# Performance work log

Measured on AMD Instinct MI355X. Metric: run time of the kernel, lower is better.

## Reference

```python
import jax, jax.numpy as jnp
import numpy as np

H = 512  # hidden_size


def setup_inputs() -> dict:
    key = jax.random.key(0)
    ks = jax.random.split(key, 7)
    B, T, I = 256, 512, 3
    s = 1.0 / np.sqrt(H)
    return {
        "x": jax.random.normal(ks[0], (B, T, I), dtype=jnp.float32),
        "W_ih": jax.random.uniform(ks[1], (4 * H, I), dtype=jnp.float32, minval=-s, maxval=s),
        "W_hh": jax.random.uniform(ks[2], (4 * H, H), dtype=jnp.float32, minval=-s, maxval=s),
        "b_ih": jax.random.uniform(ks[3], (4 * H,), dtype=jnp.float32, minval=-s, maxval=s),
        "b_hh": jax.random.uniform(ks[4], (4 * H,), dtype=jnp.float32, minval=-s, maxval=s),
        "fc_w": jax.random.uniform(ks[5], (1, H), dtype=jnp.float32, minval=-s, maxval=s),
        "fc_b": jax.random.uniform(ks[6], (1,), dtype=jnp.float32, minval=-s, maxval=s),
    }


def _lstm_last_h(x, W_ih, W_hh, b_ih, b_hh):
    B = x.shape[0]
    # precompute input contribution for all timesteps: [B, T, 4H]
    x_gates = jnp.einsum('bti,gi->btg', x, W_ih) + (b_ih + b_hh)
    h0 = jnp.zeros((B, H), dtype=x.dtype)
    c0 = jnp.zeros((B, H), dtype=x.dtype)

    def step(carry, xg):
        h, c = carry
        gates = xg + h @ W_hh.T  # [B, 4H]
        i, f, g, o = jnp.split(gates, 4, axis=-1)  # torch order: i, f, g, o
        i = jax.nn.sigmoid(i)
        f = jax.nn.sigmoid(f)
        g = jnp.tanh(g)
        o = jax.nn.sigmoid(o)
        c_new = f * c + i * g
        h_new = o * jnp.tanh(c_new)
        return (h_new, c_new), None

    (h_last, _), _ = jax.lax.scan(step, (h0, c0), jnp.swapaxes(x_gates, 0, 1))
    return h_last  # [B, H]


def reference(x, W_ih, W_hh, b_ih, b_hh, fc_w, fc_b):
    h_last = _lstm_last_h(x, W_ih, W_hh, b_ih, b_hh)
    return h_last @ fc_w.T + fc_b  # [B, 1]
```

## Files before the change

kernel.cpp:

```cpp
#include <hip/hip_runtime.h>


#define Hh   512
#define Bsz  256
#define Tt   512

#define MB   32
#define HS   16
#define NROW 64
#define NTHR 512
#define NWG  256

typedef float    f32x4 __attribute__((ext_vector_type(4)));
typedef _Float16 f16x8 __attribute__((ext_vector_type(8)));
typedef unsigned long long u64;

#define PLANE_ELE (Bsz * Hh)
#define PLANES   3
#define BAR_OFF  (PLANES * PLANE_ELE * 2)
#define CTRL_UINTS 4096

__device__ __forceinline__ float sigm(float v)  { return 1.0f / (1.0f + __expf(-v)); }
__device__ __forceinline__ float tanhx(float v) { return 2.0f / (1.0f + __expf(-2.0f * v)) - 1.0f; }

__device__ __forceinline__ ushort f2h(float f) {
  return __builtin_bit_cast(ushort, (_Float16)f);
}
__device__ __forceinline__ float h2f(ushort u) {
  return (float)__builtin_bit_cast(_Float16, u);
}

#define GLOAD(dst, base, imm)                                            \
  asm volatile("global_load_dwordx4 %0, %1, off offset:%c2 sc0 sc1"      \
               : "=v"(dst) : "v"(base), "i"(imm))

__global__ void init_ws(unsigned* ctrl) {
  for (int i = threadIdx.x; i < CTRL_UINTS; i += NTHR) ctrl[i] = 0u;
}

__global__ __launch_bounds__(NTHR, 2)
void lstm_kernel(const float* __restrict__ x,   const float* __restrict__ Wih,
                 const float* __restrict__ Whh, const float* __restrict__ bih,
                 const float* __restrict__ bhh, const float* __restrict__ fcw,
                 const float* __restrict__ fcb, float* __restrict__ out,
                 char* __restrict__ ws)
{
  const int tid = threadIdx.x;
  const int wg  = blockIdx.x;
  const int bb  = wg & 7;
  const int hb  = wg >> 3;
  const int j0  = hb * HS;
  const int b0  = bb * MB;

  ushort*   hpl   = (ushort*)ws;
  unsigned* flags = (unsigned*)(ws + BAR_OFF) + bb * 512;

  __shared__ ushort whiF[4 * 16 * 64 * 8];
  __shared__ ushort wloF[4 * 16 * 64 * 8];
  __shared__ float  gates2[2][4][MB][20];
  __shared__ float  wih_s[NROW][3];
  __shared__ float  bsum[NROW];
  __shared__ float  xs[MB][3];

  if (tid < NROW) {
    int qq = tid >> 4, jj = tid & 15;
    int grow = qq * Hh + j0 + jj;
    wih_s[tid][0] = Wih[grow * 3 + 0];
    wih_s[tid][1] = Wih[grow * 3 + 1];
    wih_s[tid][2] = Wih[grow * 3 + 2];
    bsum[tid] = bih[grow] + bhh[grow];
  }

  for (int idx = tid; idx < NROW * 64; idx += NTHR) {
    int row = idx >> 6, seg = idx & 63;
    int qq = row >> 4, jj = row & 15;
    const float* src = Whh + (size_t)(qq * Hh + j0 + jj) * Hh + seg * 8;
    float4 w0 = *(const float4*)(src);
    float4 w1 = *(const float4*)(src + 4);
    float wv[8] = {w0.x, w0.y, w0.z, w0.w, w1.x, w1.y, w1.z, w1.w};
    unsigned uhi[4], ulo[4];
    #pragma unroll
    for (int p = 0; p < 4; ++p) {
      ushort h0 = f2h(wv[2*p]);
      ushort h1 = f2h(wv[2*p+1]);
      ushort l0 = f2h((wv[2*p]   - h2f(h0)) * 1024.0f);
      ushort l1 = f2h((wv[2*p+1] - h2f(h1)) * 1024.0f);
      uhi[p] = (unsigned)h0 | ((unsigned)h1 << 16);
      ulo[p] = (unsigned)l0 | ((unsigned)l1 << 16);
    }
    int kblk = seg >> 2, lkk = seg & 3;
    int dst = ((qq * 16 + kblk) * 64 + lkk * 16 + jj) * 8;
    *(uint4*)&whiF[dst] = make_uint4(uhi[0], uhi[1], uhi[2], uhi[3]);
    *(uint4*)&wloF[dst] = make_uint4(ulo[0], ulo[1], ulo[2], ulo[3]);
  }

  {
    int b = tid >> 4, jj = tid & 15;
    size_t o = (size_t)(b0 + b) * Hh + j0 + jj;
    __hip_atomic_store(&hpl[o], (ushort)0, __ATOMIC_RELAXED, __HIP_MEMORY_SCOPE_AGENT);
  }
  asm volatile("s_waitcnt vmcnt(0)" ::: "memory");
  __syncthreads();
  if (tid == 0) {
    unsigned fv = 1u;
    asm volatile("global_store_dword %0, %1, off sc0 sc1"
                 :: "v"(flags + hb * 16), "v"(fv) : "memory");
  }

  const int l   = tid & 63;
  const int wid = tid >> 6;
  const int m   = wid >> 2;
  const int ks  = wid & 3;
  const int lm  = l & 15;
  const int lk  = l >> 4;

  const size_t aoff = (size_t)(b0 + m * 16 + lm) * Hh + ks * 128 + lk * 8;
  const int    wq0  = ks * 2048 + l * 8;

  const int cb = tid >> 4;
  const int cj = tid & 15;
  float c_state = 0.0f;

  int rd = 0, wr = 1;
  for (int t = 0; t < Tt; ++t) {
    {
      const unsigned tq = (unsigned)(t + 1);
      const unsigned tw = (unsigned)t;
      if (wid == 0) {
        unsigned v = 0xFFFFFFFFu;
        const unsigned* fp = flags + (l & 31) * 16;
        for (;;) {
          if (l < 32)
            asm volatile("global_load_dword %0, %1, off sc0 sc1" : "=v"(v) : "v"(fp) : "memory");
          asm volatile("s_waitcnt vmcnt(0)" ::: "memory");
          unsigned need = ((l & 31) < 8) ? tq : tw;
          if (__all((int)(v >= need))) break;
          __builtin_amdgcn_s_sleep(2);
        }
      } else {
        unsigned v = 0xFFFFFFFFu;
        const unsigned* fp = flags + (ks * 8 + (l & 7)) * 16;
        for (;;) {
          if (l < 8)
            asm volatile("global_load_dword %0, %1, off sc0 sc1" : "=v"(v) : "v"(fp) : "memory");
          asm volatile("s_waitcnt vmcnt(0)" ::: "memory");
          if (__all((int)(v >= tq))) break;
          __builtin_amdgcn_s_sleep(2);
        }
      }
    }

    if (tid < MB * 3) {
      int b = tid / 3, ii = tid - b * 3;
      xs[b][ii] = x[(size_t)(b0 + b) * (Tt * 3) + t * 3 + ii];
    }

    const char* pH = (const char*)(hpl + (size_t)rd * PLANE_ELE + aoff);
    f32x4 AH[4];
    GLOAD(AH[0], pH, 0);  GLOAD(AH[1], pH, 64);  GLOAD(AH[2], pH, 128); GLOAD(AH[3], pH, 192);
    asm volatile("s_waitcnt vmcnt(0)" ::: "memory");
    __builtin_amdgcn_sched_barrier(0);

    f32x4 h0 = {0,0,0,0}, h1 = {0,0,0,0}, h2 = {0,0,0,0}, h3 = {0,0,0,0};
    f32x4 l0 = {0,0,0,0}, l1 = {0,0,0,0}, l2 = {0,0,0,0}, l3 = {0,0,0,0};
    #pragma unroll
    for (int u = 0; u < 4; ++u) {
      f16x8 ah = __builtin_bit_cast(f16x8, AH[u]);
      const int fo = wq0 + u * 512;
      {
        f16x8 bh = *(const f16x8*)&whiF[0 * 8192 + fo];
        f16x8 bl = *(const f16x8*)&wloF[0 * 8192 + fo];
        h0 = __builtin_amdgcn_mfma_f32_16x16x32_f16(ah, bh, h0, 0, 0, 0);
        l0 = __builtin_amdgcn_mfma_f32_16x16x32_f16(ah, bl, l0, 0, 0, 0);
      }
      {
        f16x8 bh = *(const f16x8*)&whiF[1 * 8192 + fo];
        f16x8 bl = *(const f16x8*)&wloF[1 * 8192 + fo];
        h1 = __builtin_amdgcn_mfma_f32_16x16x32_f16(ah, bh, h1, 0, 0, 0);
        l1 = __builtin_amdgcn_mfma_f32_16x16x32_f16(ah, bl, l1, 0, 0, 0);
      }
      {
        f16x8 bh = *(const f16x8*)&whiF[2 * 8192 + fo];
        f16x8 bl = *(const f16x8*)&wloF[2 * 8192 + fo];
        h2 = __builtin_amdgcn_mfma_f32_16x16x32_f16(ah, bh, h2, 0, 0, 0);
        l2 = __builtin_amdgcn_mfma_f32_16x16x32_f16(ah, bl, l2, 0, 0, 0);
      }
      {
        f16x8 bh = *(const f16x8*)&whiF[3 * 8192 + fo];
        f16x8 bl = *(const f16x8*)&wloF[3 * 8192 + fo];
        h3 = __builtin_amdgcn_mfma_f32_16x16x32_f16(ah, bh, h3, 0, 0, 0);
        l3 = __builtin_amdgcn_mfma_f32_16x16x32_f16(ah, bl, l3, 0, 0, 0);
      }
    }
    const float ls = 1.0f / 1024.0f;
    f32x4 acc0 = h0 + l0 * ls;
    f32x4 acc1 = h1 + l1 * ls;
    f32x4 acc2 = h2 + l2 * ls;
    f32x4 acc3 = h3 + l3 * ls;

    const int rrow = m * 16 + lk * 4;
    if (ks < 2) {
      #pragma unroll
      for (int r = 0; r < 4; ++r) {
        gates2[ks][0][rrow + r][lm] = acc0[r];
        gates2[ks][1][rrow + r][lm] = acc1[r];
        gates2[ks][2][rrow + r][lm] = acc2[r];
        gates2[ks][3][rrow + r][lm] = acc3[r];
      }
    }
    __syncthreads();
    if (ks >= 2) {
      #pragma unroll
      for (int r = 0; r < 4; ++r) {
        gates2[ks - 2][0][rrow + r][lm] += acc0[r];
        gates2[ks - 2][1][rrow + r][lm] += acc1[r];
        gates2[ks - 2][2][rrow + r][lm] += acc2[r];
        gates2[ks - 2][3][rrow + r][lm] += acc3[r];
      }
    }
    __syncthreads();

    {
      float xv0 = xs[cb][0], xv1 = xs[cb][1], xv2 = xs[cb][2];
      float pre[4];
      #pragma unroll
      for (int qq = 0; qq < 4; ++qq) {
        int r = qq * 16 + cj;
        pre[qq] = gates2[0][qq][cb][cj] + gates2[1][qq][cb][cj] + bsum[r]
                + xv0 * wih_s[r][0] + xv1 * wih_s[r][1] + xv2 * wih_s[r][2];
      }
      float ig = sigm(pre[0]), fg = sigm(pre[1]);
      float gg = tanhx(pre[2]), og = sigm(pre[3]);
      c_state = fg * c_state + ig * gg;
      float hv = og * tanhx(c_state);
      unsigned uhw = f2h(hv);
      size_t ho = (size_t)wr * PLANE_ELE + (size_t)(b0 + cb) * Hh + j0 + cj;
      asm volatile("global_store_short %0, %1, off sc0 sc1" :: "v"(hpl + ho), "v"(uhw));
    }

    asm volatile("s_waitcnt vmcnt(0)" ::: "memory");
    __syncthreads();
    if (tid == 0) {
      unsigned fv = (unsigned)(t + 2);
      asm volatile("global_store_dword %0, %1, off sc0 sc1"
                   :: "v"(flags + hb * 16), "v"(fv) : "memory");
    }

    rd = wr;
    wr = (wr == 2) ? 0 : wr + 1;
  }

  if (hb == 0) {
    if (tid < 64) {
      unsigned v = 0xFFFFFFFFu;
      const unsigned* fp = flags + (l & 31) * 16;
      const unsigned tgt = (unsigned)(Tt + 1);
      for (;;) {
        if (l < 32)
          asm volatile("global_load_dword %0, %1, off sc0 sc1" : "=v"(v) : "v"(fp) : "memory");
        asm volatile("s_waitcnt vmcnt(0)" ::: "memory");
        if (__all((int)(v >= tgt))) break;
        __builtin_amdgcn_s_sleep(2);
      }
    }
    __syncthreads();

    const u64* Hf = (const u64*)(hpl + (size_t)rd * PLANE_ELE);
    int b = tid >> 4, lj = tid & 15;
    float p = 0.0f;
    for (int jq = lj; jq < Hh / 4; jq += 16) {
      size_t o = (size_t)(b0 + b) * (Hh / 4) + jq;
      u64 uh = __hip_atomic_load(Hf + o, __ATOMIC_RELAXED, __HIP_MEMORY_SCOPE_AGENT);
      #pragma unroll
      for (int e = 0; e < 4; ++e)
        p += h2f((ushort)(uh >> (16 * e))) * fcw[4 * jq + e];
    }
    __syncthreads();
    ((float*)gates2)[tid] = p;
    __syncthreads();
    if (lj == 0) {
      float s = 0.0f;
      #pragma unroll
      for (int r = 0; r < 16; ++r) s += ((float*)gates2)[(b << 4) + r];
      out[b0 + b] = s + fcb[0];
    }
  }
}

extern "C" void kernel_launch(void* const* d_in, const int* in_sizes, int n_in,
                              void* d_out, int out_size, void* d_ws, size_t ws_size,
                              hipStream_t stream) {
  const float* x   = (const float*)d_in[0];
  const float* Wih = (const float*)d_in[1];
  const float* Whh = (const float*)d_in[2];
  const float* bih = (const float*)d_in[3];
  const float* bhh = (const float*)d_in[4];
  const float* fcw = (const float*)d_in[5];
  const float* fcb = (const float*)d_in[6];
  float* out = (float*)d_out;
  char*  ws  = (char*)d_ws;

  hipLaunchKernelGGL(init_ws, dim3(1), dim3(NTHR), 0, stream,
                     (unsigned*)(ws + BAR_OFF));
  hipLaunchKernelGGL(lstm_kernel, dim3(NWG), dim3(NTHR), 0, stream,
                     x, Wih, Whh, bih, bhh, fcw, fcb, out, ws);
}
```

Before: 1.834 ms.

## Keep W_hh fragments in registers, drop split-fp16 low part, retile to 16x32

Retiles the persistent LSTM grid from 8 batch groups x 32 hidden slices to 16 batch groups x 16 hidden slices of 32 units each. The recurrent weights now live as single fp16 MFMA fragments in each thread's registers instead of hi/lo fp16 pairs in LDS. This halves the MFMA count and removes the per-step LDS weight reads. Each wave handles a K-slice of 64 and the partial results are reduced through LDS across 8 waves. Dropping the low-order weight correction lowers accuracy, and the larger register footprint may hurt occupancy or cause spills.

```diff
diff --git a/kernel.cpp b/kernel.cpp
--- a/kernel.cpp
+++ b/kernel.cpp
@@ -5,9 +5,9 @@
 #define Bsz  256
 #define Tt   512
 
-#define MB   32
-#define HS   16
-#define NROW 64
+#define MB   16
+#define HS   32
+#define NROW 128
 #define NTHR 512
 #define NWG  256
 
@@ -23,11 +23,11 @@
 __device__ __forceinline__ float sigm(float v)  { return 1.0f / (1.0f + __expf(-v)); }
 __device__ __forceinline__ float tanhx(float v) { return 2.0f / (1.0f + __expf(-2.0f * v)) - 1.0f; }
 
+__device__ __forceinline__ float h2f(ushort u) {
+  return (float)__builtin_bit_cast(_Float16, u);
+}
 __device__ __forceinline__ ushort f2h(float f) {
   return __builtin_bit_cast(ushort, (_Float16)f);
-}
-__device__ __forceinline__ float h2f(ushort u) {
-  return (float)__builtin_bit_cast(_Float16, u);
 }
 
 #define GLOAD(dst, base, imm)                                            \
@@ -47,23 +47,21 @@
 {
   const int tid = threadIdx.x;
   const int wg  = blockIdx.x;
-  const int bb  = wg & 7;
-  const int hb  = wg >> 3;
+  const int bb  = wg & 15;
+  const int hb  = wg >> 4;
   const int j0  = hb * HS;
   const int b0  = bb * MB;
 
   ushort*   hpl   = (ushort*)ws;
-  unsigned* flags = (unsigned*)(ws + BAR_OFF) + bb * 512;
-
-  __shared__ ushort whiF[4 * 16 * 64 * 8];
-  __shared__ ushort wloF[4 * 16 * 64 * 8];
-  __shared__ float  gates2[2][4][MB][20];
-  __shared__ float  wih_s[NROW][3];
-  __shared__ float  bsum[NROW];
-  __shared__ float  xs[MB][3];
+  unsigned* flags = (unsigned*)(ws + BAR_OFF) + bb * 256;
+
+  __shared__ float gates2[4][NROW][17];
+  __shared__ float wih_s[NROW][3];
+  __shared__ float bsum[NROW];
+  __shared__ float xs[MB][3];
 
   if (tid < NROW) {
-    int qq = tid >> 4, jj = tid & 15;
+    int qq = tid >> 5, jj = tid & 31;
     int grow = qq * Hh + j0 + jj;
     wih_s[tid][0] = Wih[grow * 3 + 0];
     wih_s[tid][1] = Wih[grow * 3 + 1];
@@ -71,32 +69,34 @@
     bsum[tid] = bih[grow] + bhh[grow];
   }
 
-  for (int idx = tid; idx < NROW * 64; idx += NTHR) {
-    int row = idx >> 6, seg = idx & 63;
-    int qq = row >> 4, jj = row & 15;
-    const float* src = Whh + (size_t)(qq * Hh + j0 + jj) * Hh + seg * 8;
-    float4 w0 = *(const float4*)(src);
-    float4 w1 = *(const float4*)(src + 4);
-    float wv[8] = {w0.x, w0.y, w0.z, w0.w, w1.x, w1.y, w1.z, w1.w};
-    unsigned uhi[4], ulo[4];
+  const int l   = tid & 63;
+  const int ks  = tid >> 6;
+  const int lm  = l & 15;
+  const int lk  = l >> 4;
+
+  f16x8 wfrag[8][2];
+  #pragma unroll
+  for (int rb = 0; rb < 8; ++rb) {
     #pragma unroll
-    for (int p = 0; p < 4; ++p) {
-      ushort h0 = f2h(wv[2*p]);
-      ushort h1 = f2h(wv[2*p+1]);
-      ushort l0 = f2h((wv[2*p]   - h2f(h0)) * 1024.0f);
-      ushort l1 = f2h((wv[2*p+1] - h2f(h1)) * 1024.0f);
-      uhi[p] = (unsigned)h0 | ((unsigned)h1 << 16);
-      ulo[p] = (unsigned)l0 | ((unsigned)l1 << 16);
-    }
-    int kblk = seg >> 2, lkk = seg & 3;
-    int dst = ((qq * 16 + kblk) * 64 + lkk * 16 + jj) * 8;
-    *(uint4*)&whiF[dst] = make_uint4(uhi[0], uhi[1], uhi[2], uhi[3]);
-    *(uint4*)&wloF[dst] = make_uint4(ulo[0], ulo[1], ulo[2], ulo[3]);
+    for (int kb = 0; kb < 2; ++kb) {
+      int rr = rb * 16 + lm;
+      int grow = (rr >> 5) * Hh + j0 + (rr & 31);
+      int col = (ks * 2 + kb) * 32 + lk * 8;
+      const float* wsrc = Whh + (size_t)grow * Hh + col;
+      float4 wa = *(const float4*)(wsrc);
+      float4 wb = *(const float4*)(wsrc + 4);
+      f16x8 f;
+      f[0] = (_Float16)wa.x; f[1] = (_Float16)wa.y;
+      f[2] = (_Float16)wa.z; f[3] = (_Float16)wa.w;
+      f[4] = (_Float16)wb.x; f[5] = (_Float16)wb.y;
+      f[6] = (_Float16)wb.z; f[7] = (_Float16)wb.w;
+      wfrag[rb][kb] = f;
+    }
   }
 
   {
-    int b = tid >> 4, jj = tid & 15;
-    size_t o = (size_t)(b0 + b) * Hh + j0 + jj;
+    int cb0 = tid >> 5, cj0 = tid & 31;
+    size_t o = (size_t)(b0 + cb0) * Hh + j0 + cj0;
     __hip_atomic_store(&hpl[o], (ushort)0, __ATOMIC_RELAXED, __HIP_MEMORY_SCOPE_AGENT);
   }
   asm volatile("s_waitcnt vmcnt(0)" ::: "memory");
@@ -107,18 +107,10 @@
                  :: "v"(flags + hb * 16), "v"(fv) : "memory");
   }
 
-  const int l   = tid & 63;
-  const int wid = tid >> 6;
-  const int m   = wid >> 2;
-  const int ks  = wid & 3;
-  const int lm  = l & 15;
-  const int lk  = l >> 4;
-
-  const size_t aoff = (size_t)(b0 + m * 16 + lm) * Hh + ks * 128 + lk * 8;
-  const int    wq0  = ks * 2048 + l * 8;
-
-  const int cb = tid >> 4;
-  const int cj = tid & 15;
+  const size_t aoff = (size_t)(b0 + lm) * Hh + ks * 64 + lk * 8;
+
+  const int cb = tid >> 5;
+  const int cj = tid & 31;
   float c_state = 0.0f;
 
   int rd = 0, wr = 1;
@@ -126,22 +118,22 @@
     {
       const unsigned tq = (unsigned)(t + 1);
       const unsigned tw = (unsigned)t;
-      if (wid == 0) {
+      if (ks == 0) {
         unsigned v = 0xFFFFFFFFu;
-        const unsigned* fp = flags + (l & 31) * 16;
+        const unsigned* fp = flags + (l & 15) * 16;
         for (;;) {
-          if (l < 32)
+          if (l < 16)
             asm volatile("global_load_dword %0, %1, off sc0 sc1" : "=v"(v) : "v"(fp) : "memory");
           asm volatile("s_waitcnt vmcnt(0)" ::: "memory");
-          unsigned need = ((l & 31) < 8) ? tq : tw;
+          unsigned need = ((l & 15) < 2) ? tq : tw;
           if (__all((int)(v >= need))) break;
           __builtin_amdgcn_s_sleep(2);
         }
       } else {
         unsigned v = 0xFFFFFFFFu;
-        const unsigned* fp = flags + (ks * 8 + (l & 7)) * 16;
+        const unsigned* fp = flags + (ks * 2 + (l & 1)) * 16;
         for (;;) {
-          if (l < 8)
+          if (l < 2)
             asm volatile("global_load_dword %0, %1, off sc0 sc1" : "=v"(v) : "v"(fp) : "memory");
           asm volatile("s_waitcnt vmcnt(0)" ::: "memory");
           if (__all((int)(v >= tq))) break;
@@ -156,67 +148,36 @@
     }
 
     const char* pH = (const char*)(hpl + (size_t)rd * PLANE_ELE + aoff);
-    f32x4 AH[4];
-    GLOAD(AH[0], pH, 0);  GLOAD(AH[1], pH, 64);  GLOAD(AH[2], pH, 128); GLOAD(AH[3], pH, 192);
+    f32x4 AH[2];
+    GLOAD(AH[0], pH, 0);  GLOAD(AH[1], pH, 64);
     asm volatile("s_waitcnt vmcnt(0)" ::: "memory");
     __builtin_amdgcn_sched_barrier(0);
 
-    f32x4 h0 = {0,0,0,0}, h1 = {0,0,0,0}, h2 = {0,0,0,0}, h3 = {0,0,0,0};
-    f32x4 l0 = {0,0,0,0}, l1 = {0,0,0,0}, l2 = {0,0,0,0}, l3 = {0,0,0,0};
+    f32x4 acc[8];
     #pragma unroll
-    for (int u = 0; u < 4; ++u) {
-      f16x8 ah = __builtin_bit_cast(f16x8, AH[u]);
-      const int fo = wq0 + u * 512;
-      {
-        f16x8 bh = *(const f16x8*)&whiF[0 * 8192 + fo];
-        f16x8 bl = *(const f16x8*)&wloF[0 * 8192 + fo];
-        h0 = __builtin_amdgcn_mfma_f32_16x16x32_f16(ah, bh, h0, 0, 0, 0);
-        l0 = __builtin_amdgcn_mfma_f32_16x16x32_f16(ah, bl, l0, 0, 0, 0);
-      }
-      {
-        f16x8 bh = *(const f16x8*)&whiF[1 * 8192 + fo];
-        f16x8 bl = *(const f16x8*)&wloF[1 * 8192 + fo];
-        h1 = __builtin_amdgcn_mfma_f32_16x16x32_f16(ah, bh, h1, 0, 0, 0);
-        l1 = __builtin_amdgcn_mfma_f32_16x16x32_f16(ah, bl, l1, 0, 0, 0);
-      }
-      {
-        f16x8 bh = *(const f16x8*)&whiF[2 * 8192 + fo];
-        f16x8 bl = *(const f16x8*)&wloF[2 * 8192 + fo];
-        h2 = __builtin_amdgcn_mfma_f32_16x16x32_f16(ah, bh, h2, 0, 0, 0);
-        l2 = __builtin_amdgcn_mfma_f32_16x16x32_f16(ah, bl, l2, 0, 0, 0);
-      }
-      {
-        f16x8 bh = *(const f16x8*)&whiF[3 * 8192 + fo];
-        f16x8 bl = *(const f16x8*)&wloF[3 * 8192 + fo];
-        h3 = __builtin_amdgcn_mfma_f32_16x16x32_f16(ah, bh, h3, 0, 0, 0);
-        l3 = __builtin_amdgcn_mfma_f32_16x16x32_f16(ah, bl, l3, 0, 0, 0);
-      }
-    }
-    const float ls = 1.0f / 1024.0f;
-    f32x4 acc0 = h0 + l0 * ls;
-    f32x4 acc1 = h1 + l1 * ls;
-    f32x4 acc2 = h2 + l2 * ls;
-    f32x4 acc3 = h3 + l3 * ls;
-
-    const int rrow = m * 16 + lk * 4;
-    if (ks < 2) {
-      #pragma unroll
-      for (int r = 0; r < 4; ++r) {
-        gates2[ks][0][rrow + r][lm] = acc0[r];
-        gates2[ks][1][rrow + r][lm] = acc1[r];
-        gates2[ks][2][rrow + r][lm] = acc2[r];
-        gates2[ks][3][rrow + r][lm] = acc3[r];
-      }
-    }
-    __syncthreads();
-    if (ks >= 2) {
-      #pragma unroll
-      for (int r = 0; r < 4; ++r) {
-        gates2[ks - 2][0][rrow + r][lm] += acc0[r];
-        gates2[ks - 2][1][rrow + r][lm] += acc1[r];
-        gates2[ks - 2][2][rrow + r][lm] += acc2[r];
-        gates2[ks - 2][3][rrow + r][lm] += acc3[r];
-      }
+    for (int rb = 0; rb < 8; ++rb) acc[rb] = (f32x4){0.f, 0.f, 0.f, 0.f};
+    #pragma unroll
+    for (int kb = 0; kb < 2; ++kb) {
+      f16x8 ah = __builtin_bit_cast(f16x8, AH[kb]);
+      #pragma unroll
+      for (int rb = 0; rb < 8; ++rb)
+        acc[rb] = __builtin_amdgcn_mfma_f32_16x16x32_f16(ah, wfrag[rb][kb], acc[rb], 0, 0, 0);
+    }
+
+    if (ks < 4) {
+      #pragma unroll
+      for (int rb = 0; rb < 8; ++rb)
+        #pragma unroll
+        for (int r = 0; r < 4; ++r)
+          gates2[ks][rb * 16 + lm][lk * 4 + r] = acc[rb][r];
+    }
+    __syncthreads();
+    if (ks >= 4) {
+      #pragma unroll
+      for (int rb = 0; rb < 8; ++rb)
+        #pragma unroll
+        for (int r = 0; r < 4; ++r)
+          gates2[ks - 4][rb * 16 + lm][lk * 4 + r] += acc[rb][r];
     }
     __syncthreads();
 
@@ -225,9 +186,10 @@
       float pre[4];
       #pragma unroll
       for (int qq = 0; qq < 4; ++qq) {
-        int r = qq * 16 + cj;
-        pre[qq] = gates2[0][qq][cb][cj] + gates2[1][qq][cb][cj] + bsum[r]
-                + xv0 * wih_s[r][0] + xv1 * wih_s[r][1] + xv2 * wih_s[r][2];
+        int rrq = qq * 32 + cj;
+        pre[qq] = gates2[0][rrq][cb] + gates2[1][rrq][cb]
+                + gates2[2][rrq][cb] + gates2[3][rrq][cb] + bsum[rrq]
+                + xv0 * wih_s[rrq][0] + xv1 * wih_s[rrq][1] + xv2 * wih_s[rrq][2];
       }
       float ig = sigm(pre[0]), fg = sigm(pre[1]);
       float gg = tanhx(pre[2]), og = sigm(pre[3]);
@@ -253,10 +215,10 @@
   if (hb == 0) {
     if (tid < 64) {
       unsigned v = 0xFFFFFFFFu;
-      const unsigned* fp = flags + (l & 31) * 16;
+      const unsigned* fp = flags + (l & 15) * 16;
       const unsigned tgt = (unsigned)(Tt + 1);
       for (;;) {
-        if (l < 32)
+        if (l < 16)
           asm volatile("global_load_dword %0, %1, off sc0 sc1" : "=v"(v) : "v"(fp) : "memory");
         asm volatile("s_waitcnt vmcnt(0)" ::: "memory");
         if (__all((int)(v >= tgt))) break;
@@ -266,9 +228,9 @@
     __syncthreads();
 
     const u64* Hf = (const u64*)(hpl + (size_t)rd * PLANE_ELE);
-    int b = tid >> 4, lj = tid & 15;
+    int b = tid >> 5, lj = tid & 31;
     float p = 0.0f;
-    for (int jq = lj; jq < Hh / 4; jq += 16) {
+    for (int jq = lj; jq < Hh / 4; jq += 32) {
       size_t o = (size_t)(b0 + b) * (Hh / 4) + jq;
       u64 uh = __hip_atomic_load(Hf + o, __ATOMIC_RELAXED, __HIP_MEMORY_SCOPE_AGENT);
       #pragma unroll
@@ -281,7 +243,7 @@
     if (lj == 0) {
       float s = 0.0f;
       #pragma unroll
-      for (int r = 0; r < 16; ++r) s += ((float*)gates2)[(b << 4) + r];
+      for (int r = 0; r < 32; ++r) s += ((float*)gates2)[(b << 5) + r];
       out[b0 + b] = s + fcb[0];
     }
   }
```

New measurement: 1.698 ms. 1.08x faster.
